# Optimization experiments

Measured on AMD Instinct MI355X. Metric: run time of the kernel, lower is better.

## Reference

```python
import jax, jax.numpy as jnp
import numpy as np

D_MODEL = 1024
NUM_HEADS = 16
HEAD_DIM = D_MODEL // NUM_HEADS
B, S = 2, 2048


def setup_inputs() -> dict:
    key = jax.random.key(0)
    ks = jax.random.split(key, 8)
    scale = 1.0 / np.sqrt(D_MODEL)
    inp = {
        "query": jax.random.normal(ks[0], (B, S, D_MODEL), jnp.float32),
        "key": jax.random.normal(ks[1], (B, S, D_MODEL), jnp.float32),
        "value": jax.random.normal(ks[2], (B, S, D_MODEL), jnp.float32),
        # causal mask, broadcastable over batch and heads
        "mask": jnp.tril(jnp.ones((S, S), dtype=bool))[None, None, :, :],
        # torch nn.Linear weights: y = x @ W.T (+ b)
        "Wq": jax.random.normal(ks[3], (D_MODEL, D_MODEL), jnp.float32) * scale,
        "Wk": jax.random.normal(ks[4], (D_MODEL, D_MODEL), jnp.float32) * scale,
        "Wv": jax.random.normal(ks[5], (D_MODEL, D_MODEL), jnp.float32) * scale,
        "Wo": jax.random.normal(ks[6], (D_MODEL, D_MODEL), jnp.float32) * scale,
        "bo": jax.random.normal(ks[7], (D_MODEL,), jnp.float32) * scale,
    }
    return inp


def _split_heads(x):
    b, s, _ = x.shape
    return x.reshape(b, s, NUM_HEADS, HEAD_DIM).transpose(0, 2, 1, 3)  # [B,H,S,Dh]


def reference(query, key, value, mask, Wq, Wk, Wv, Wo, bo):
    q = _split_heads(query @ Wq.T)
    k = _split_heads(key @ Wk.T)
    v = _split_heads(value @ Wv.T)
    scores = jnp.einsum("bhqd,bhkd->bhqk", q, k) / jnp.sqrt(jnp.float32(HEAD_DIM))
    scores = jnp.where(mask, scores, jnp.float32(-jnp.inf))
    attn = jax.nn.softmax(scores, axis=-1)
    out = jnp.einsum("bhqk,bhkd->bhqd", attn, v)  # [B,H,S,Dh]
    out = out.transpose(0, 2, 1, 3).reshape(query.shape[0], q.shape[2], D_MODEL)
    return out @ Wo.T + bo
```

## Files before the change

kernel.cpp:

```cpp
#include <hip/hip_runtime.h>
#include <hip/hip_bf16.h>

#define DM   1024
#define NH   16
#define HD   64
#define SEQ  2048
#define BATCH 2
#define MTOT (BATCH*SEQ)

typedef unsigned short u16;
typedef __attribute__((ext_vector_type(8))) short bf16x8;
typedef __attribute__((ext_vector_type(4))) float f32x4;

#define SC2F 0.1803368801111464f

__device__ __forceinline__ float bf2f(u16 h) {
  union { unsigned int i; float f; } u; u.i = ((unsigned int)h) << 16; return u.f;
}
__device__ __forceinline__ u16 f2bf(float f) {
  union { float f; unsigned int i; } u; u.f = f;
  unsigned int r = u.i + 0x7fffu + ((u.i >> 16) & 1u);
  return (u16)(r >> 16);
}
__device__ __forceinline__ unsigned int pk2(float lo, float hi) {
  union { float f; unsigned int u; } a, b; a.f = lo; b.f = hi;
  return ((a.u + 0x8000u) >> 16) | ((b.u + 0x8000u) & 0xFFFF0000u);
}

__global__ void detect_dtype(const u16* __restrict__ q, int* __restrict__ flag) {
  const int lane = threadIdx.x & 63;
  int cnt = 0;
  for (int i = 0; i < 8; i++) {
    int e = (q[i*64 + lane] >> 7) & 0xFF;
    unsigned long long m = __ballot(e >= 0x6E && e <= 0x8F);
    cnt += __popcll(m);
  }
  if (lane == 0) *flag = (cnt >= 400) ? 1 : 0;
}

__device__ __forceinline__ uint4 load8_bf16(const void* base, size_t elemOff, bool isf32) {
  if (!isf32) return *(const uint4*)((const u16*)base + elemOff);
  const float* f = (const float*)base + elemOff;
  f32x4 a = *(const f32x4*)f;
  f32x4 b = *(const f32x4*)(f + 4);
  union { u16 h[8]; uint4 v; } r;
  r.h[0]=f2bf(a[0]); r.h[1]=f2bf(a[1]); r.h[2]=f2bf(a[2]); r.h[3]=f2bf(a[3]);
  r.h[4]=f2bf(b[0]); r.h[5]=f2bf(b[1]); r.h[6]=f2bf(b[2]); r.h[7]=f2bf(b[3]);
  return r.v;
}

__global__ __launch_bounds__(256) void prep(
    const void* __restrict__ q, const void* __restrict__ k, const void* __restrict__ v,
    const void* __restrict__ wq, const void* __restrict__ wk, const void* __restrict__ wv,
    const void* __restrict__ wo, const void* __restrict__ bo,
    u16* __restrict__ Xq, u16* __restrict__ Xk, u16* __restrict__ Xv,
    u16* __restrict__ Wqb, u16* __restrict__ Wkb, u16* __restrict__ Wvb, u16* __restrict__ Wob,
    float* __restrict__ biasf, const int* __restrict__ dflag)
{
  const bool isf32 = (*dflag == 0);
  const int z = blockIdx.z;
  if (z == 7) {
    if (blockIdx.x == 0) {
      for (int i = threadIdx.x; i < DM; i += 256)
        biasf[i] = isf32 ? ((const float*)bo)[i] : bf2f(((const u16*)bo)[i]);
    }
    return;
  }
  const void* src; u16* dst; size_t n;
  switch (z) {
    case 0: src=q;  dst=Xq;  n=(size_t)MTOT*DM; break;
    case 1: src=k;  dst=Xk;  n=(size_t)MTOT*DM; break;
    case 2: src=v;  dst=Xv;  n=(size_t)MTOT*DM; break;
    case 3: src=wq; dst=Wqb; n=(size_t)DM*DM;   break;
    case 4: src=wk; dst=Wkb; n=(size_t)DM*DM;   break;
    case 5: src=wv; dst=Wvb; n=(size_t)DM*DM;   break;
    default: src=wo; dst=Wob; n=(size_t)DM*DM;  break;
  }
  const size_t stride = (size_t)gridDim.x * 256 * 8;
  for (size_t i = ((size_t)blockIdx.x * 256 + threadIdx.x) * 8; i < n; i += stride)
    *(uint4*)(dst + i) = load8_bf16(src, i, isf32);
}

__device__ __forceinline__ void gld16(const u16* g, u16* l) {
  __builtin_amdgcn_global_load_lds(
      (const __attribute__((address_space(1))) void*)g,
      (__attribute__((address_space(3))) void*)l, 16, 0, 0);
}

template<int MODE>
__global__ __launch_bounds__(256) void gemm128(
    const u16* __restrict__ X0, const u16* __restrict__ X1, const u16* __restrict__ X2,
    const u16* __restrict__ W0, const u16* __restrict__ W1, const u16* __restrict__ W2,
    const float* __restrict__ biasf,
    u16* __restrict__ F0, u16* __restrict__ F1, u16* __restrict__ F2,
    void* __restrict__ outP, const int* __restrict__ dflag)
{
  __shared__ u16 As[128*32];
  __shared__ u16 Bs[128*32];

  const u16* X; const u16* W; u16* outF = nullptr; int zz = 0;
  if (MODE == 0) {
    zz = blockIdx.z;
    X    = (zz==0) ? X0 : ((zz==1) ? X1 : X2);
    W    = (zz==0) ? W0 : ((zz==1) ? W1 : W2);
    outF = (zz==0) ? F0 : ((zz==1) ? F1 : F2);
  } else { X = X0; W = W0; }

  const int tid = threadIdx.x;
  const int wave = tid >> 6, lane = tid & 63, quad = lane >> 4, l16 = lane & 15;
  const int wr = wave >> 1, wc = wave & 1;
  const int m0 = blockIdx.y * 128, n0 = blockIdx.x * 128;

  const int sg = ((lane & 3) ^ ((lane >> 3) & 3)) * 8;
  const int rS = wave*32 + (lane >> 2);
  const u16* gA0 = X + (size_t)(m0 + rS)*DM + sg;
  const u16* gA1 = X + (size_t)(m0 + rS + 16)*DM + sg;
  const u16* gB0 = W + (size_t)(n0 + rS)*DM + sg;
  const u16* gB1 = W + (size_t)(n0 + rS + 16)*DM + sg;
  u16* lA0 = &As[wave*1024];
  u16* lA1 = &As[wave*1024 + 512];
  u16* lB0 = &Bs[wave*1024];
  u16* lB1 = &Bs[wave*1024 + 512];

  const int xslot8 = (quad ^ ((l16 >> 1) & 3)) * 8;

  f32x4 acc[4][4];
#pragma unroll
  for (int i = 0; i < 4; i++)
#pragma unroll
    for (int j = 0; j < 4; j++) { acc[i][j][0]=0.f; acc[i][j][1]=0.f; acc[i][j][2]=0.f; acc[i][j][3]=0.f; }

  for (int k0 = 0; k0 < DM; k0 += 32) {
    __syncthreads();
    gld16(gA0 + k0, lA0);
    gld16(gA1 + k0, lA1);
    gld16(gB0 + k0, lB0);
    gld16(gB1 + k0, lB1);
    __syncthreads();

    bf16x8 af[4], bfr[4];
#pragma unroll
    for (int fr = 0; fr < 4; fr++)
      af[fr] = *(const bf16x8*)&As[(wr*64 + fr*16 + l16)*32 + xslot8];
#pragma unroll
    for (int fc = 0; fc < 4; fc++)
      bfr[fc] = *(const bf16x8*)&Bs[(wc*64 + fc*16 + l16)*32 + xslot8];
#pragma unroll
    for (int fr = 0; fr < 4; fr++)
#pragma unroll
      for (int fc = 0; fc < 4; fc++)
        acc[fr][fc] = __builtin_amdgcn_mfma_f32_16x16x32_bf16(af[fr], bfr[fc], acc[fr][fc], 0, 0, 0);
  }

  if (MODE == 0 && zz == 2) {
    __shared__ u16 Ts[64*128];
    const int bb = m0 >> 11;
    const int s0 = m0 & (SEQ-1);
#pragma unroll
    for (int p = 0; p < 2; p++) {
      __syncthreads();
      if (wc == p) {
#pragma unroll
        for (int fr = 0; fr < 4; fr++) {
#pragma unroll
          for (int fc = 0; fc < 4; fc++) {
            const int dl = fc*16 + l16;
            const int sb = wr*64 + fr*16 + quad*4;
            const int slot = (sb >> 3) ^ (dl & 15);
            u16* rowp = &Ts[dl*128 + slot*8 + (sb & 7)];
            *(unsigned int*)(rowp)     = pk2(acc[fr][fc][0], acc[fr][fc][1]);
            *(unsigned int*)(rowp + 2) = pk2(acc[fr][fc][2], acc[fr][fc][3]);
          }
        }
      }
      __syncthreads();
      const int dl2 = tid >> 2, ch4 = tid & 3;
      const int hh = (n0 + p*64) >> 6;
      u16* dst = outF + ((size_t)(bb*NH + hh)*HD + dl2)*SEQ + s0 + ch4*32;
#pragma unroll
      for (int j = 0; j < 4; j++) {
        const int slot = (ch4*4 + j) ^ (dl2 & 15);
        *(uint4*)&dst[j*8] = *(const uint4*)&Ts[dl2*128 + slot*8];
      }
    }
    return;
  }

  const bool isf32 = (MODE == 1) && (*dflag == 0);
#pragma unroll
  for (int fr = 0; fr < 4; fr++) {
#pragma unroll
    for (int rr = 0; rr < 4; rr++) {
      const int m = m0 + wr*64 + fr*16 + quad*4 + rr;
#pragma unroll
      for (int fc = 0; fc < 4; fc++) {
        const int n = n0 + wc*64 + fc*16 + l16;
        float vv = acc[fr][fc][rr];
        if (MODE == 0) {
          if (zz == 0) vv *= SC2F;
          const int b = m >> 11, s = m & (SEQ-1), h = n >> 6, d = n & (HD-1);
          outF[((size_t)(b*NH + h)*SEQ + s)*HD + d] = f2bf(vv);
        } else {
          vv += biasf[n];
          if (isf32) ((float*)outP)[(size_t)m*DM + n] = vv;
          else       ((u16*)outP)[(size_t)m*DM + n]   = f2bf(vv);
        }
      }
    }
  }
}

__global__ __launch_bounds__(256) void attn_mfma(
    const u16* __restrict__ Qb, const u16* __restrict__ Kb,
    const u16* __restrict__ Vtb,
    u16* __restrict__ Opart, float* __restrict__ mlpart)
{
  __shared__ u16 Qs[64*64];
  __shared__ u16 Ks[64*64];
  __shared__ u16 Vs[64*64];
  __shared__ u16 Ps[4][16][72];

  const int bh = blockIdx.x;
  const int pr = blockIdx.y, z = blockIdx.z;
  const u16* Qp = Qb  + (size_t)bh * SEQ * HD;
  const u16* Kp = Kb  + (size_t)bh * SEQ * HD;
  const u16* Vp = Vtb + (size_t)bh * HD * SEQ;

  const int tid  = threadIdx.x;
  const int wave = tid >> 6, lane = tid & 63, quad = lane >> 4, l16 = lane & 15;

  const int i0 = wave*128 + lane, i1 = i0 + 64;
  const int r0 = i0 >> 3, c0 = (i0 & 7) ^ (r0 & 7);
  const int r1 = i1 >> 3, c1 = (i1 & 7) ^ (r1 & 7);
  const int kq_off0 = r0*HD + c0*8;
  const int kq_off1 = r1*HD + c1*8;
  const int v_off0  = r0*SEQ + c0*8;
  const int v_off1  = r1*SEQ + c1*8;
  u16* ldsQ0 = &Qs[wave*1024]; u16* ldsQ1 = &Qs[wave*1024 + 512];
  u16* ldsK0 = &Ks[wave*1024]; u16* ldsK1 = &Ks[wave*1024 + 512];
  u16* ldsV0 = &Vs[wave*1024]; u16* ldsV1 = &Vs[wave*1024 + 512];

  const int l7 = l16 & 7;

  for (int ph = 0; ph < 2; ph++) {
    const int qt = ph ? (31 - pr) : pr;
    const int n = qt + 1, half = (n + 1) >> 1;
    const int klo = z ? half : 0, khi = z ? n : half;
    const int q0 = qt * 64;

    __syncthreads();
    gld16(Qp + q0*HD + kq_off0, ldsQ0);
    gld16(Qp + q0*HD + kq_off1, ldsQ1);

    const int ql = wave*16 + l16;
    const int qg = q0 + ql;
    f32x4 O[4];
#pragma unroll
    for (int u = 0; u < 4; u++) { O[u][0]=0.f; O[u][1]=0.f; O[u][2]=0.f; O[u][3]=0.f; }
    float mi = -__builtin_inff(), li = 0.f;

    for (int kt = klo; kt < khi; kt++) {
      __syncthreads();
      gld16(Kp + kt*(64*HD) + kq_off0, ldsK0);
      gld16(Kp + kt*(64*HD) + kq_off1, ldsK1);
      gld16(Vp + kt*64 + v_off0, ldsV0);
      gld16(Vp + kt*64 + v_off1, ldsV1);
      __syncthreads();

      f32x4 st[4];
#pragma unroll
      for (int t = 0; t < 4; t++) { st[t][0]=0.f; st[t][1]=0.f; st[t][2]=0.f; st[t][3]=0.f; }
#pragma unroll
      for (int s = 0; s < 2; s++) {
        const int ch = s*4 + quad;
        bf16x8 bq = *(const bf16x8*)&Qs[(ql*8 + (ch ^ l7))*8];
#pragma unroll
        for (int t = 0; t < 4; t++) {
          bf16x8 ak = *(const bf16x8*)&Ks[((t*16 + l16)*8 + (ch ^ l7))*8];
          st[t] = __builtin_amdgcn_mfma_f32_16x16x32_bf16(ak, bq, st[t], 0, 0, 0);
        }
      }

      float v[4][4];
#pragma unroll
      for (int t = 0; t < 4; t++)
#pragma unroll
        for (int r = 0; r < 4; r++) v[t][r] = st[t][r];
      if (kt == qt) {
#pragma unroll
        for (int t = 0; t < 4; t++)
#pragma unroll
          for (int r = 0; r < 4; r++)
            if (kt*64 + t*16 + quad*4 + r > qg) v[t][r] = -__builtin_inff();
      }
      float mx = v[0][0];
#pragma unroll
      for (int t = 0; t < 4; t++)
#pragma unroll
        for (int r = 0; r < 4; r++) mx = fmaxf(mx, v[t][r]);
      mx = fmaxf(mx, __shfl_xor(mx, 16));
      mx = fmaxf(mx, __shfl_xor(mx, 32));
      const float nm = fmaxf(mi, mx);
      const float al = exp2f(mi - nm);
      float ps = 0.f;
#pragma unroll
      for (int t = 0; t < 4; t++) {
        float p0 = exp2f(v[t][0] - nm), p1 = exp2f(v[t][1] - nm);
        float p2 = exp2f(v[t][2] - nm), p3 = exp2f(v[t][3] - nm);
        ps += (p0 + p1) + (p2 + p3);
        uint2 u2; u2.x = pk2(p0, p1); u2.y = pk2(p2, p3);
        *(uint2*)&Ps[wave][l16][t*16 + quad*4] = u2;
      }
      ps += __shfl_xor(ps, 16);
      ps += __shfl_xor(ps, 32);
      li = li * al + ps;
      mi = nm;
#pragma unroll
      for (int u = 0; u < 4; u++) {
        O[u][0] *= al; O[u][1] *= al; O[u][2] *= al; O[u][3] *= al;
      }
      __asm__ volatile("s_waitcnt lgkmcnt(0)" ::: "memory");

#pragma unroll
      for (int s = 0; s < 2; s++) {
        const int ch = s*4 + quad;
        bf16x8 bp = *(const bf16x8*)&Ps[wave][l16][s*32 + quad*8];
#pragma unroll
        for (int u = 0; u < 4; u++) {
          bf16x8 av = *(const bf16x8*)&Vs[((u*16 + l16)*8 + (ch ^ l7))*8];
          O[u] = __builtin_amdgcn_mfma_f32_16x16x32_bf16(av, bp, O[u], 0, 0, 0);
        }
      }
    }

    const int pi = (bh*32 + qt)*2 + z;
    u16* op = Opart + (size_t)pi*4096 + ql*64;
#pragma unroll
    for (int u = 0; u < 4; u++) {
      uint2 u2; u2.x = pk2(O[u][0], O[u][1]); u2.y = pk2(O[u][2], O[u][3]);
      *(uint2*)&op[u*16 + quad*4] = u2;
    }
    if (quad == 0) {
      float2 ml2; ml2.x = mi; ml2.y = li;
      *(float2*)&mlpart[(size_t)pi*128 + ql*2] = ml2;
    }
  }
}

__global__ __launch_bounds__(64) void attn_merge(
    const u16* __restrict__ Opart, const float* __restrict__ mlpart,
    u16* __restrict__ aO)
{
  const int g = blockIdx.x;
  const int bh = g & 31, qt = g >> 5;
  const int b = bh >> 4, h = bh & 15;
  const int t = threadIdx.x;
  const int pi0 = (bh*32 + qt)*2, pi1 = pi0 + 1;

  const float2 ml0 = *(const float2*)&mlpart[(size_t)pi0*128 + t*2];
  const float2 ml1 = *(const float2*)&mlpart[(size_t)pi1*128 + t*2];
  const float M = fmaxf(ml0.x, ml1.x);
  float w0 = exp2f(ml0.x - M), w1 = exp2f(ml1.x - M);
  const float inv = 1.0f / (w0*ml0.y + w1*ml1.y);
  w0 *= inv; w1 *= inv;

  const u16* o0 = Opart + (size_t)pi0*4096 + t*64;
  const u16* o1 = Opart + (size_t)pi1*4096 + t*64;
  u16* out = aO + (size_t)(b*SEQ + qt*64 + t)*DM + h*HD;
#pragma unroll
  for (int d0 = 0; d0 < 64; d0 += 8) {
    union { uint4 v; u16 h[8]; } a, c; union { uint4 v; u16 h[8]; } bb;
    a.v  = *(const uint4*)&o0[d0];
    bb.v = *(const uint4*)&o1[d0];
#pragma unroll
    for (int j = 0; j < 8; j += 2) {
      float x0 = w0*bf2f(a.h[j])   + w1*bf2f(bb.h[j]);
      float x1 = w0*bf2f(a.h[j+1]) + w1*bf2f(bb.h[j+1]);
      unsigned int pk = pk2(x0, x1);
      c.h[j] = (u16)(pk & 0xFFFF); c.h[j+1] = (u16)(pk >> 16);
    }
    *(uint4*)&out[d0] = c.v;
  }
}

extern "C" void kernel_launch(void* const* d_in, const int* in_sizes, int n_in,
                              void* d_out, int out_size, void* d_ws, size_t ws_size,
                              hipStream_t stream) {
  const void* q  = d_in[0];
  const void* k  = d_in[1];
  const void* v  = d_in[2];
  const void* wq = d_in[4];
  const void* wk = d_in[5];
  const void* wv = d_in[6];
  const void* wo = d_in[7];
  const void* bo = d_in[8];

  const size_t TX = (size_t)MTOT*DM;
  const size_t TW = (size_t)DM*DM;
  u16* ws  = (u16*)d_ws;
  u16* Xq  = ws;
  u16* Xk  = ws + TX;
  u16* Xv  = ws + 2*TX;
  u16* Wqb = ws + 3*TX;
  u16* Wkb = Wqb + TW;
  u16* Wvb = Wqb + 2*TW;
  u16* Wob = Wqb + 3*TW;
  u16* Qw  = ws + 3*TX + 4*TW;
  u16* Kw  = Qw + TX;
  u16* Vt  = Qw + 2*TX;
  u16*   Opart  = Xk;
  float* mlpart = (float*)Wqb;
  u16*   aO     = Xq;
  float* biasf  = (float*)(Qw + 3*TX);
  int*   fl     = (int*)(biasf + DM);

  dim3 blk(256);
  detect_dtype<<<1, 64, 0, stream>>>((const u16*)q, fl);
  prep<<<dim3(512, 1, 8), blk, 0, stream>>>(q, k, v, wq, wk, wv, wo, bo,
      Xq, Xk, Xv, Wqb, Wkb, Wvb, Wob, biasf, fl);
  gemm128<0><<<dim3(DM/128, MTOT/128, 3), blk, 0, stream>>>(
      Xq, Xk, Xv, Wqb, Wkb, Wvb, nullptr, Qw, Kw, Vt, nullptr, fl);
  attn_mfma<<<dim3(BATCH*NH, 16, 2), blk, 0, stream>>>(Qw, Kw, Vt, Opart, mlpart);
  attn_merge<<<dim3(32*32), dim3(64), 0, stream>>>(Opart, mlpart, aO);
  gemm128<1><<<dim3(DM/128, MTOT/128, 1), blk, 0, stream>>>(
      aO, nullptr, nullptr, Wob, nullptr, nullptr, biasf, nullptr, nullptr, nullptr, d_out, fl);
}
```

Before: 254.5 us.

## Fold dtype detection into prep, retile output GEMM, swap grid axes

Removes the separate dtype-detect launch: every prep block now samples the query bits itself and block z=7 writes the flag for later kernels. Splits the templated GEMM into a QKV kernel and an output-projection kernel. The output kernel uses 128x64 tiles so it launches twice as many blocks and fills more CUs. Both GEMM grids swap the M and N axes, which changes the order blocks are scheduled and how they share cache.

```diff
diff --git a/kernel.cpp b/kernel.cpp
--- a/kernel.cpp
+++ b/kernel.cpp
@@ -25,17 +25,6 @@
 __device__ __forceinline__ unsigned int pk2(float lo, float hi) {
   union { float f; unsigned int u; } a, b; a.f = lo; b.f = hi;
   return ((a.u + 0x8000u) >> 16) | ((b.u + 0x8000u) & 0xFFFF0000u);
-}
-
-__global__ void detect_dtype(const u16* __restrict__ q, int* __restrict__ flag) {
-  const int lane = threadIdx.x & 63;
-  int cnt = 0;
-  for (int i = 0; i < 8; i++) {
-    int e = (q[i*64 + lane] >> 7) & 0xFF;
-    unsigned long long m = __ballot(e >= 0x6E && e <= 0x8F);
-    cnt += __popcll(m);
-  }
-  if (lane == 0) *flag = (cnt >= 400) ? 1 : 0;
 }
 
 __device__ __forceinline__ uint4 load8_bf16(const void* base, size_t elemOff, bool isf32) {
@@ -55,13 +44,27 @@
     const void* __restrict__ wo, const void* __restrict__ bo,
     u16* __restrict__ Xq, u16* __restrict__ Xk, u16* __restrict__ Xv,
     u16* __restrict__ Wqb, u16* __restrict__ Wkb, u16* __restrict__ Wvb, u16* __restrict__ Wob,
-    float* __restrict__ biasf, const int* __restrict__ dflag)
+    float* __restrict__ biasf, int* __restrict__ flag_out)
 {
-  const bool isf32 = (*dflag == 0);
+  const int tid = threadIdx.x;
+  __shared__ int cnts[4];
+  {
+    const u16* qs = (const u16*)q;
+    int e0 = (qs[tid*2]   >> 7) & 0xFF;
+    int e1 = (qs[tid*2+1] >> 7) & 0xFF;
+    int c = ((e0 >= 0x6E && e0 <= 0x8F) ? 1 : 0) + ((e1 >= 0x6E && e1 <= 0x8F) ? 1 : 0);
+    c += __shfl_xor(c, 1);  c += __shfl_xor(c, 2);  c += __shfl_xor(c, 4);
+    c += __shfl_xor(c, 8);  c += __shfl_xor(c, 16); c += __shfl_xor(c, 32);
+    if ((tid & 63) == 0) cnts[tid >> 6] = c;
+  }
+  __syncthreads();
+  const bool isf32 = (cnts[0] + cnts[1] + cnts[2] + cnts[3]) < 400;
+
   const int z = blockIdx.z;
   if (z == 7) {
     if (blockIdx.x == 0) {
-      for (int i = threadIdx.x; i < DM; i += 256)
+      if (tid == 0) *flag_out = isf32 ? 0 : 1;
+      for (int i = tid; i < DM; i += 256)
         biasf[i] = isf32 ? ((const float*)bo)[i] : bf2f(((const u16*)bo)[i]);
     }
     return;
@@ -77,7 +80,7 @@
     default: src=wo; dst=Wob; n=(size_t)DM*DM;  break;
   }
   const size_t stride = (size_t)gridDim.x * 256 * 8;
-  for (size_t i = ((size_t)blockIdx.x * 256 + threadIdx.x) * 8; i < n; i += stride)
+  for (size_t i = ((size_t)blockIdx.x * 256 + tid) * 8; i < n; i += stride)
     *(uint4*)(dst + i) = load8_bf16(src, i, isf32);
 }
 
@@ -87,29 +90,23 @@
       (__attribute__((address_space(3))) void*)l, 16, 0, 0);
 }
 
-template<int MODE>
-__global__ __launch_bounds__(256) void gemm128(
+__global__ __launch_bounds__(256) void gemm_qkv(
     const u16* __restrict__ X0, const u16* __restrict__ X1, const u16* __restrict__ X2,
     const u16* __restrict__ W0, const u16* __restrict__ W1, const u16* __restrict__ W2,
-    const float* __restrict__ biasf,
-    u16* __restrict__ F0, u16* __restrict__ F1, u16* __restrict__ F2,
-    void* __restrict__ outP, const int* __restrict__ dflag)
+    u16* __restrict__ F0, u16* __restrict__ F1, u16* __restrict__ F2)
 {
   __shared__ u16 As[128*32];
   __shared__ u16 Bs[128*32];
 
-  const u16* X; const u16* W; u16* outF = nullptr; int zz = 0;
-  if (MODE == 0) {
-    zz = blockIdx.z;
-    X    = (zz==0) ? X0 : ((zz==1) ? X1 : X2);
-    W    = (zz==0) ? W0 : ((zz==1) ? W1 : W2);
-    outF = (zz==0) ? F0 : ((zz==1) ? F1 : F2);
-  } else { X = X0; W = W0; }
+  const int zz = blockIdx.z;
+  const u16* X = (zz==0) ? X0 : ((zz==1) ? X1 : X2);
+  const u16* W = (zz==0) ? W0 : ((zz==1) ? W1 : W2);
+  u16* outF    = (zz==0) ? F0 : ((zz==1) ? F1 : F2);
 
   const int tid = threadIdx.x;
   const int wave = tid >> 6, lane = tid & 63, quad = lane >> 4, l16 = lane & 15;
   const int wr = wave >> 1, wc = wave & 1;
-  const int m0 = blockIdx.y * 128, n0 = blockIdx.x * 128;
+  const int m0 = blockIdx.x * 128, n0 = blockIdx.y * 128;
 
   const int sg = ((lane & 3) ^ ((lane >> 3) & 3)) * 8;
   const int rS = wave*32 + (lane >> 2);
@@ -152,7 +149,7 @@
         acc[fr][fc] = __builtin_amdgcn_mfma_f32_16x16x32_bf16(af[fr], bfr[fc], acc[fr][fc], 0, 0, 0);
   }
 
-  if (MODE == 0 && zz == 2) {
+  if (zz == 2) {
     __shared__ u16 Ts[64*128];
     const int bb = m0 >> 11;
     const int s0 = m0 & (SEQ-1);
@@ -186,7 +183,6 @@
     return;
   }
 
-  const bool isf32 = (MODE == 1) && (*dflag == 0);
 #pragma unroll
   for (int fr = 0; fr < 4; fr++) {
 #pragma unroll
@@ -196,15 +192,78 @@
       for (int fc = 0; fc < 4; fc++) {
         const int n = n0 + wc*64 + fc*16 + l16;
         float vv = acc[fr][fc][rr];
-        if (MODE == 0) {
-          if (zz == 0) vv *= SC2F;
-          const int b = m >> 11, s = m & (SEQ-1), h = n >> 6, d = n & (HD-1);
-          outF[((size_t)(b*NH + h)*SEQ + s)*HD + d] = f2bf(vv);
-        } else {
-          vv += biasf[n];
-          if (isf32) ((float*)outP)[(size_t)m*DM + n] = vv;
-          else       ((u16*)outP)[(size_t)m*DM + n]   = f2bf(vv);
-        }
+        if (zz == 0) vv *= SC2F;
+        const int b = m >> 11, s = m & (SEQ-1), h = n >> 6, d = n & (HD-1);
+        outF[((size_t)(b*NH + h)*SEQ + s)*HD + d] = f2bf(vv);
+      }
+    }
+  }
+}
+
+__global__ __launch_bounds__(256) void gemm_out(
+    const u16* __restrict__ X, const u16* __restrict__ W,
+    const float* __restrict__ biasf, void* __restrict__ outP,
+    const int* __restrict__ dflag)
+{
+  __shared__ u16 As[128*32];
+  __shared__ u16 Bs[64*32];
+
+  const int tid = threadIdx.x;
+  const int wave = tid >> 6, lane = tid & 63, quad = lane >> 4, l16 = lane & 15;
+  const int wr = wave >> 1, wc = wave & 1;
+  const int m0 = blockIdx.x * 128, n0 = blockIdx.y * 64;
+
+  const int sg = ((lane & 3) ^ ((lane >> 3) & 3)) * 8;
+  const int rA = wave*32 + (lane >> 2);
+  const int rB = wave*16 + (lane >> 2);
+  const u16* gA0 = X + (size_t)(m0 + rA)*DM + sg;
+  const u16* gA1 = X + (size_t)(m0 + rA + 16)*DM + sg;
+  const u16* gB0 = W + (size_t)(n0 + rB)*DM + sg;
+  u16* lA0 = &As[wave*1024];
+  u16* lA1 = &As[wave*1024 + 512];
+  u16* lB0 = &Bs[wave*512];
+
+  const int xslot8 = (quad ^ ((l16 >> 1) & 3)) * 8;
+
+  f32x4 acc[4][2];
+#pragma unroll
+  for (int i = 0; i < 4; i++)
+#pragma unroll
+    for (int j = 0; j < 2; j++) { acc[i][j][0]=0.f; acc[i][j][1]=0.f; acc[i][j][2]=0.f; acc[i][j][3]=0.f; }
+
+  for (int k0 = 0; k0 < DM; k0 += 32) {
+    __syncthreads();
+    gld16(gA0 + k0, lA0);
+    gld16(gA1 + k0, lA1);
+    gld16(gB0 + k0, lB0);
+    __syncthreads();
+
+    bf16x8 af[4], bfr[2];
+#pragma unroll
+    for (int fr = 0; fr < 4; fr++)
+      af[fr] = *(const bf16x8*)&As[(wr*64 + fr*16 + l16)*32 + xslot8];
+#pragma unroll
+    for (int fc = 0; fc < 2; fc++)
+      bfr[fc] = *(const bf16x8*)&Bs[(wc*32 + fc*16 + l16)*32 + xslot8];
+#pragma unroll
+    for (int fr = 0; fr < 4; fr++)
+#pragma unroll
+      for (int fc = 0; fc < 2; fc++)
+        acc[fr][fc] = __builtin_amdgcn_mfma_f32_16x16x32_bf16(af[fr], bfr[fc], acc[fr][fc], 0, 0, 0);
+  }
+
+  const bool isf32 = (*dflag == 0);
+#pragma unroll
+  for (int fr = 0; fr < 4; fr++) {
+#pragma unroll
+    for (int rr = 0; rr < 4; rr++) {
+      const int m = m0 + wr*64 + fr*16 + quad*4 + rr;
+#pragma unroll
+      for (int fc = 0; fc < 2; fc++) {
+        const int n = n0 + wc*32 + fc*16 + l16;
+        float vv = acc[fr][fc][rr] + biasf[n];
+        if (isf32) ((float*)outP)[(size_t)m*DM + n] = vv;
+        else       ((u16*)outP)[(size_t)m*DM + n]   = f2bf(vv);
       }
     }
   }
@@ -415,13 +474,11 @@
   int*   fl     = (int*)(biasf + DM);
 
   dim3 blk(256);
-  detect_dtype<<<1, 64, 0, stream>>>((const u16*)q, fl);
   prep<<<dim3(512, 1, 8), blk, 0, stream>>>(q, k, v, wq, wk, wv, wo, bo,
       Xq, Xk, Xv, Wqb, Wkb, Wvb, Wob, biasf, fl);
-  gemm128<0><<<dim3(DM/128, MTOT/128, 3), blk, 0, stream>>>(
-      Xq, Xk, Xv, Wqb, Wkb, Wvb, nullptr, Qw, Kw, Vt, nullptr, fl);
+  gemm_qkv<<<dim3(MTOT/128, DM/128, 3), blk, 0, stream>>>(
+      Xq, Xk, Xv, Wqb, Wkb, Wvb, Qw, Kw, Vt);
   attn_mfma<<<dim3(BATCH*NH, 16, 2), blk, 0, stream>>>(Qw, Kw, Vt, Opart, mlpart);
   attn_merge<<<dim3(32*32), dim3(64), 0, stream>>>(Opart, mlpart, aO);
-  gemm128<1><<<dim3(DM/128, MTOT/128, 1), blk, 0, stream>>>(
-      aO, nullptr, nullptr, Wob, nullptr, nullptr, biasf, nullptr, nullptr, nullptr, d_out, fl);
-}
+  gemm_out<<<dim3(MTOT/128, DM/64), blk, 0, stream>>>(aO, Wob, biasf, d_out, fl);
+}
```

Measured after the change: 243.6 us. 1.04x faster.
